# Performance work log

Measured on AMD Instinct MI355X. Metric: run time of the kernel, lower is better.

Reference implementation:

```python
import jax, jax.numpy as jnp
import numpy as np

N = 50000      # nodes
E = 800000     # edges
M = 1000000    # total subgraph membership rows
D = 128        # atom_fea_len
ED = 64        # nbr_fea_len
H = 8          # heads
C = D // H     # per-head dim


def _ln(x, g, b, eps=1e-5):
    mu = x.mean(-1, keepdims=True)
    var = ((x - mu) ** 2).mean(-1, keepdims=True)
    return (x - mu) / jnp.sqrt(var + eps) * g + b


def setup_inputs() -> dict:
    key = jax.random.key(0)
    ks = jax.random.split(key, 16)
    s = 0.05
    inp = {
        "x": jax.random.normal(ks[0], (N, D), jnp.float32),
        "edge_index": jax.random.randint(ks[1], (2, E), 0, N, jnp.int32),
        "edge_attr": jax.random.normal(ks[2], (E, ED), jnp.float32),
        "sub_nodes": jax.random.randint(ks[3], (M,), 0, N, jnp.int32),
        "sub_indicator": jax.random.randint(ks[4], (M,), 0, N, jnp.int32),
        # TransformerConv params (PyG: lin_query/key/value, lin_edge, lin_skip, all with bias)
        "Wq": jax.random.normal(ks[5], (D, D), jnp.float32) * s,
        "bq": jnp.zeros((D,), jnp.float32),
        "Wk": jax.random.normal(ks[6], (D, D), jnp.float32) * s,
        "bk": jnp.zeros((D,), jnp.float32),
        "Wv": jax.random.normal(ks[7], (D, D), jnp.float32) * s,
        "bv": jnp.zeros((D,), jnp.float32),
        "We": jax.random.normal(ks[8], (ED, D), jnp.float32) * s,
        "be": jnp.zeros((D,), jnp.float32),
        "Ws": jax.random.normal(ks[9], (D, D), jnp.float32) * s,
        "bs": jnp.zeros((D,), jnp.float32),
        # subgraph_norm
        "sn_g": jnp.ones((D,), jnp.float32),
        "sn_b": jnp.zeros((D,), jnp.float32),
        # subgraph_proj: Linear -> SiLU -> Linear
        "p1_w": jax.random.normal(ks[10], (D, D), jnp.float32) * s,
        "p1_b": jnp.zeros((D,), jnp.float32),
        "p2_w": jax.random.normal(ks[11], (D, D), jnp.float32) * s,
        "p2_b": jnp.zeros((D,), jnp.float32),
        # out_norm
        "on_g": jnp.ones((D,), jnp.float32),
        "on_b": jnp.zeros((D,), jnp.float32),
    }
    return inp


def reference(x, edge_index, edge_attr, sub_nodes, sub_indicator,
              Wq, bq, Wk, bk, Wv, bv, We, be, Ws, bs,
              sn_g, sn_b, p1_w, p1_b, p2_w, p2_b, on_g, on_b):
    n = x.shape[0]
    src, dst = edge_index[0], edge_index[1]  # messages flow src -> dst (PyG source_to_target)

    # ---- TransformerConv ----
    q = (x @ Wq + bq).reshape(n, H, C)
    k = (x @ Wk + bk).reshape(n, H, C)
    v = (x @ Wv + bv).reshape(n, H, C)
    e = (edge_attr @ We + be).reshape(-1, H, C)       # [E,H,C]
    ke = k[src] + e                                    # edge-conditioned keys
    ve = v[src] + e                                    # edge-conditioned values
    alpha = (q[dst] * ke).sum(-1) / jnp.sqrt(jnp.asarray(C, x.dtype))  # [E,H]
    # scatter-softmax over incoming edges of each dst node
    m = jax.ops.segment_max(alpha, dst, num_segments=n)               # [N,H]
    ea = jnp.exp(alpha - m[dst])
    denom = jax.ops.segment_sum(ea, dst, num_segments=n)              # [N,H]
    num = jax.ops.segment_sum(ea[:, :, None] * ve, dst, num_segments=n)  # [N,H,C]
    attn = num / jnp.where(denom > 0, denom, 1.0)[:, :, None]
    x_trans = attn.reshape(n, H * C) + (x @ Ws + bs)   # concat heads + root skip

    # ---- subgraph branch: gather -> LayerNorm -> MLP -> scatter-mean ----
    sx = x[sub_nodes]                                  # [M,D]
    sx = _ln(sx, sn_g, sn_b)
    sx = jax.nn.silu(sx @ p1_w + p1_b) @ p2_w + p2_b
    cnt = jax.ops.segment_sum(jnp.ones((sx.shape[0],), x.dtype), sub_indicator, num_segments=n)
    sub_x = jax.ops.segment_sum(sx, sub_indicator, num_segments=n) / jnp.maximum(cnt, 1.0)[:, None]

    # ---- combine (dropout is identity in eval) ----
    out = _ln(x + x_trans + sub_x, on_g, on_b)
    return jax.nn.silu(out)
```

## Files before the change

kernel.cpp:

```cpp
#include <hip/hip_runtime.h>
#include <math.h>

#define DD 128
#define EDD 64

typedef __attribute__((ext_vector_type(8))) short bf16x8;
typedef __attribute__((ext_vector_type(4))) float f32x4;

__device__ inline unsigned short f2bf(float f) {
    unsigned int u = __float_as_uint(f);
    u += 0x7FFFu + ((u >> 16) & 1u);
    return (unsigned short)(u >> 16);
}
__device__ inline unsigned int pack2bf16(float lo, float hi) {
    return (unsigned int)f2bf(lo) | ((unsigned int)f2bf(hi) << 16);
}
__device__ inline float bflo(unsigned int u) { return __uint_as_float(u << 16); }
__device__ inline float bfhi(unsigned int u) { return __uint_as_float(u & 0xffff0000u); }

__global__ __launch_bounds__(256) void packw_kernel(const float* __restrict__ w,
                                                    unsigned short* __restrict__ packed)
{
    int idx = blockIdx.x * 256 + threadIdx.x;
    if (idx >= DD * DD) return;
    int j    = idx & 7;
    int lane = (idx >> 3) & 63;
    int kt   = (idx >> 9) & 3;
    int ncf  = idx >> 11;
    int kk  = kt * 32 + (lane >> 4) * 8 + j;
    int col = ncf * 16 + (lane & 15);
    packed[idx] = f2bf(w[kk * DD + col]);
}

__device__ inline void gemm_b(const bf16x8 af[4][2], const unsigned short* __restrict__ packB,
                              int wc, int lane, f32x4 acc[2][4])
{
    #pragma unroll
    for (int i = 0; i < 2; i++)
        #pragma unroll
        for (int j = 0; j < 4; j++) acc[i][j] = (f32x4){0.f, 0.f, 0.f, 0.f};
    #pragma unroll
    for (int kt = 0; kt < 4; kt++) {
        #pragma unroll
        for (int nc = 0; nc < 4; nc++) {
            bf16x8 b = *(const bf16x8*)&packB[(((wc * 4 + nc) * 4 + kt) * 64 + lane) * 8];
            acc[0][nc] = __builtin_amdgcn_mfma_f32_16x16x32_bf16(af[kt][0], b, acc[0][nc], 0, 0, 0);
            acc[1][nc] = __builtin_amdgcn_mfma_f32_16x16x32_bf16(af[kt][1], b, acc[1][nc], 0, 0, 0);
        }
    }
}

__global__ __launch_bounds__(256, 4) void lin4_mfma_kernel(
    const float* __restrict__ x,
    const unsigned short* __restrict__ packBq, const float* __restrict__ bq,
    const unsigned short* __restrict__ packBk, const float* __restrict__ bk,
    const unsigned short* __restrict__ packBv, const float* __restrict__ bv,
    const unsigned short* __restrict__ packBs, const float* __restrict__ bs,
    const float* __restrict__ sn_g, const float* __restrict__ sn_b,
    float* __restrict__ q, unsigned short* __restrict__ kplane, unsigned short* __restrict__ vplane,
    float* __restrict__ pre, unsigned int* __restrict__ lnx, int N)
{
    __shared__ unsigned short sxs[64 * DD];
    int tid = threadIdx.x;
    int lane = tid & 63, wid = tid >> 6;
    size_t m0 = (size_t)blockIdx.x * 64;

    {
        float g0 = sn_g[2 * lane], g1 = sn_g[2 * lane + 1];
        float b0 = sn_b[2 * lane], b1 = sn_b[2 * lane + 1];
        #pragma unroll
        for (int r = 0; r < 16; r++) {
            int tr = wid * 16 + r;
            size_t row = m0 + tr;
            float v0 = 0.f, v1 = 0.f;
            if (row < (size_t)N) {
                float2 xv = *(const float2*)&x[row * DD + 2 * lane];
                v0 = xv.x; v1 = xv.y;
            }
            unsigned int uidx = ((unsigned)(tr * 64 + lane)) ^ (((unsigned)tr & 7u) << 2);
            ((unsigned int*)sxs)[uidx] = pack2bf16(v0, v1);
            float s1 = v0 + v1, s2 = v0 * v0 + v1 * v1;
            #pragma unroll
            for (int o = 32; o >= 1; o >>= 1) { s1 += __shfl_xor(s1, o); s2 += __shfl_xor(s2, o); }
            float mean = s1 * (1.f / DD);
            float var  = s2 * (1.f / DD) - mean * mean;
            float rs = rsqrtf(var + 1e-5f);
            if (row < (size_t)N)
                lnx[row * 64 + lane] = pack2bf16((v0 - mean) * rs * g0 + b0,
                                                 (v1 - mean) * rs * g1 + b1);
        }
    }
    __syncthreads();

    int wr = wid >> 1, wc = wid & 1;
    int rA = wr * 32 + (lane & 15);
    int kb = (lane >> 4) * 8;

    bf16x8 af[4][2];
    #pragma unroll
    for (int kt = 0; kt < 4; kt++) {
        int k0 = kt * 32 + kb;
        af[kt][0] = *(const bf16x8*)&sxs[((rA)      * DD + k0) ^ ((rA & 7) << 3)];
        int rA1 = rA + 16;
        af[kt][1] = *(const bf16x8*)&sxs[((rA1)     * DD + k0) ^ ((rA1 & 7) << 3)];
    }

    f32x4 acc[2][4];
    int colb = wc * 64 + (lane & 15);
    int jrow = (lane >> 4) * 4;

    gemm_b(af, packBq, wc, lane, acc);
    #pragma unroll
    for (int mrf = 0; mrf < 2; mrf++) {
        int rbase = wr * 32 + mrf * 16 + jrow;
        #pragma unroll
        for (int nc = 0; nc < 4; nc++) {
            int col = colb + nc * 16;
            float bias = bq[col];
            #pragma unroll
            for (int j = 0; j < 4; j++) {
                size_t row = m0 + rbase + j;
                if (row < (size_t)N) q[row * DD + col] = acc[mrf][nc][j] + bias;
            }
        }
    }
    gemm_b(af, packBk, wc, lane, acc);
    #pragma unroll
    for (int mrf = 0; mrf < 2; mrf++) {
        int rbase = wr * 32 + mrf * 16 + jrow;
        #pragma unroll
        for (int nc = 0; nc < 4; nc++) {
            int col = colb + nc * 16;
            float bias = bk[col];
            #pragma unroll
            for (int j = 0; j < 4; j++) {
                size_t row = m0 + rbase + j;
                if (row < (size_t)N) kplane[row * DD + col] = f2bf(acc[mrf][nc][j] + bias);
            }
        }
    }
    gemm_b(af, packBv, wc, lane, acc);
    #pragma unroll
    for (int mrf = 0; mrf < 2; mrf++) {
        int rbase = wr * 32 + mrf * 16 + jrow;
        #pragma unroll
        for (int nc = 0; nc < 4; nc++) {
            int col = colb + nc * 16;
            float bias = bv[col];
            #pragma unroll
            for (int j = 0; j < 4; j++) {
                size_t row = m0 + rbase + j;
                if (row < (size_t)N) vplane[row * DD + col] = f2bf(acc[mrf][nc][j] + bias);
            }
        }
    }
    gemm_b(af, packBs, wc, lane, acc);
    #pragma unroll
    for (int mrf = 0; mrf < 2; mrf++) {
        int rbase = wr * 32 + mrf * 16 + jrow;
        #pragma unroll
        for (int nc = 0; nc < 4; nc++) {
            int col = colb + nc * 16;
            float bias = bs[col];
            #pragma unroll
            for (int j = 0; j < 4; j++) {
                size_t row = m0 + rbase + j;
                if (row < (size_t)N)
                    pre[row * DD + col] = x[row * DD + col] + acc[mrf][nc][j] + bias;
            }
        }
    }
}

__global__ __launch_bounds__(256, 4) void mlpnode_kernel(
    const unsigned int* __restrict__ lnx,
    const unsigned short* __restrict__ packB1, const float* __restrict__ p1b,
    const unsigned short* __restrict__ packB2, const float* __restrict__ p2b,
    unsigned short* __restrict__ fnode, int N)
{
    __shared__ unsigned short sxs[64 * DD];
    int tid = threadIdx.x;
    int lane = tid & 63, wid = tid >> 6;
    size_t m0 = (size_t)blockIdx.x * 64;

    #pragma unroll
    for (int r = 0; r < 16; r++) {
        int tr = wid * 16 + r;
        size_t row = m0 + tr;
        unsigned int val = (row < (size_t)N) ? lnx[row * 64 + lane] : 0u;
        unsigned int uidx = ((unsigned)(tr * 64 + lane)) ^ (((unsigned)tr & 7u) << 2);
        ((unsigned int*)sxs)[uidx] = val;
    }
    __syncthreads();

    int wr = wid >> 1, wc = wid & 1;
    int rA = wr * 32 + (lane & 15);
    int kb = (lane >> 4) * 8;

    f32x4 acc[2][4];
    #pragma unroll
    for (int i = 0; i < 2; i++)
        #pragma unroll
        for (int j = 0; j < 4; j++) acc[i][j] = (f32x4){0.f, 0.f, 0.f, 0.f};
    #pragma unroll
    for (int kt = 0; kt < 4; kt++) {
        int k0 = kt * 32 + kb;
        bf16x8 a0 = *(const bf16x8*)&sxs[((rA)  * DD + k0) ^ ((rA & 7) << 3)];
        int rA1 = rA + 16;
        bf16x8 a1 = *(const bf16x8*)&sxs[((rA1) * DD + k0) ^ ((rA1 & 7) << 3)];
        #pragma unroll
        for (int nc = 0; nc < 4; nc++) {
            bf16x8 b = *(const bf16x8*)&packB1[(((wc * 4 + nc) * 4 + kt) * 64 + lane) * 8];
            acc[0][nc] = __builtin_amdgcn_mfma_f32_16x16x32_bf16(a0, b, acc[0][nc], 0, 0, 0);
            acc[1][nc] = __builtin_amdgcn_mfma_f32_16x16x32_bf16(a1, b, acc[1][nc], 0, 0, 0);
        }
    }
    __syncthreads();

    {
        float bias1[4];
        #pragma unroll
        for (int nc = 0; nc < 4; nc++) bias1[nc] = p1b[wc * 64 + nc * 16 + (lane & 15)];
        #pragma unroll
        for (int mrf = 0; mrf < 2; mrf++) {
            int rbase = wr * 32 + mrf * 16 + (lane >> 4) * 4;
            #pragma unroll
            for (int nc = 0; nc < 4; nc++) {
                int col = wc * 64 + nc * 16 + (lane & 15);
                #pragma unroll
                for (int j = 0; j < 4; j++) {
                    float h = acc[mrf][nc][j] + bias1[nc];
                    h = h / (1.f + __expf(-h));
                    int rr = rbase + j;
                    sxs[(rr * DD + col) ^ ((rr & 7) << 3)] = f2bf(h);
                }
            }
        }
    }
    __syncthreads();

    f32x4 acc2[2][4];
    #pragma unroll
    for (int i = 0; i < 2; i++)
        #pragma unroll
        for (int j = 0; j < 4; j++) acc2[i][j] = (f32x4){0.f, 0.f, 0.f, 0.f};
    #pragma unroll
    for (int kt = 0; kt < 4; kt++) {
        int k0 = kt * 32 + kb;
        bf16x8 a0 = *(const bf16x8*)&sxs[((rA)  * DD + k0) ^ ((rA & 7) << 3)];
        int rA1 = rA + 16;
        bf16x8 a1 = *(const bf16x8*)&sxs[((rA1) * DD + k0) ^ ((rA1 & 7) << 3)];
        #pragma unroll
        for (int nc = 0; nc < 4; nc++) {
            bf16x8 b = *(const bf16x8*)&packB2[(((wc * 4 + nc) * 4 + kt) * 64 + lane) * 8];
            acc2[0][nc] = __builtin_amdgcn_mfma_f32_16x16x32_bf16(a0, b, acc2[0][nc], 0, 0, 0);
            acc2[1][nc] = __builtin_amdgcn_mfma_f32_16x16x32_bf16(a1, b, acc2[1][nc], 0, 0, 0);
        }
    }

    {
        float bias2[4];
        #pragma unroll
        for (int nc = 0; nc < 4; nc++) bias2[nc] = p2b[wc * 64 + nc * 16 + (lane & 15)];
        #pragma unroll
        for (int mrf = 0; mrf < 2; mrf++) {
            int rbase = wr * 32 + mrf * 16 + (lane >> 4) * 4;
            #pragma unroll
            for (int nc = 0; nc < 4; nc++) {
                int col = wc * 64 + nc * 16 + (lane & 15);
                #pragma unroll
                for (int j = 0; j < 4; j++) {
                    size_t row = m0 + rbase + j;
                    if (row < (size_t)N)
                        fnode[row * DD + col] = f2bf(acc2[mrf][nc][j] + bias2[nc]);
                }
            }
        }
    }
}

__global__ void count_kernel(const int* __restrict__ idx, int n, int* __restrict__ cnt)
{
    int i = blockIdx.x * blockDim.x + threadIdx.x;
    int stride = gridDim.x * blockDim.x;
    for (; i < n; i += stride) atomicAdd(&cnt[idx[i]], 1);
}

__global__ __launch_bounds__(1024) void bscan_kernel(
    const int* __restrict__ inA, const int* __restrict__ inB,
    int* __restrict__ exA, int* __restrict__ exB,
    int* __restrict__ bsA, int* __restrict__ bsB, int N)
{
    const int* in = blockIdx.y ? inB : inA;
    int* ex = blockIdx.y ? exB : exA;
    int* bs = blockIdx.y ? bsB : bsA;
    __shared__ int s[1024];
    int tid = threadIdx.x;
    int i = blockIdx.x * 1024 + tid;
    int val = (i < N) ? in[i] : 0;
    s[tid] = val; __syncthreads();
    for (int off = 1; off < 1024; off <<= 1) {
        int t = (tid >= off) ? s[tid - off] : 0;
        __syncthreads();
        s[tid] += t;
        __syncthreads();
    }
    if (i < N) ex[i] = s[tid] - val;
    if (tid == 1023) bs[blockIdx.x] = s[1023];
}

__global__ void bsum_kernel(int* __restrict__ bsA, int* __restrict__ bsB,
                            int* __restrict__ indptrA, int* __restrict__ indptrB,
                            int nb, int N)
{
    int which = threadIdx.x;
    if (which < 2) {
        int* bs = which ? bsB : bsA;
        int* indptr = which ? indptrB : indptrA;
        int run = 0;
        for (int b = 0; b < nb; b++) { int v = bs[b]; bs[b] = run; run += v; }
        indptr[N] = run;
    }
}

__global__ void bfix_kernel(int* __restrict__ exA, int* __restrict__ fillA, const int* __restrict__ bsA,
                            int* __restrict__ exB, int* __restrict__ fillB, const int* __restrict__ bsB,
                            int N)
{
    int i = blockIdx.x * blockDim.x + threadIdx.x;
    if (i < N) {
        int vA = exA[i] + bsA[i >> 10];
        exA[i] = vA; fillA[i] = vA;
        int vB = exB[i] + bsB[i >> 10];
        exB[i] = vB; fillB[i] = vB;
    }
}

__global__ void escatter_kernel(const int* __restrict__ srcA, const int* __restrict__ dstA, int E,
                                int* __restrict__ fill, int2* __restrict__ spair)
{
    int i = blockIdx.x * blockDim.x + threadIdx.x;
    int stride = gridDim.x * blockDim.x;
    for (; i < E; i += stride) {
        int d = dstA[i];
        int pos = atomicAdd(&fill[d], 1);
        spair[pos] = make_int2(srcA[i], i);
    }
}

__global__ __launch_bounds__(256) void egather_kernel(
    const float* __restrict__ edge_attr, const int2* __restrict__ spair,
    unsigned int* __restrict__ ea16u, int E)
{
    size_t i = (size_t)blockIdx.x * blockDim.x + threadIdx.x;
    size_t stride = (size_t)gridDim.x * blockDim.x;
    size_t total = (size_t)E * 8;
    for (; i < total; i += stride) {
        size_t pos = i >> 3;
        int part = (int)(i & 7);
        int eid = spair[pos].y;
        const float4* s = (const float4*)&edge_attr[(size_t)eid * EDD + part * 8];
        float4 a = s[0], b = s[1];
        uint4 o;
        o.x = pack2bf16(a.x, a.y); o.y = pack2bf16(a.z, a.w);
        o.z = pack2bf16(b.x, b.y); o.w = pack2bf16(b.z, b.w);
        *(uint4*)&ea16u[pos * 32 + part * 4] = o;
    }
}

__global__ void sscatter_kernel(const int* __restrict__ sub_nodes, const int* __restrict__ sub_ind,
                                int M, int* __restrict__ sfill, int* __restrict__ snode)
{
    int i = blockIdx.x * blockDim.x + threadIdx.x;
    int stride = gridDim.x * blockDim.x;
    for (; i < M; i += stride) {
        int seg = sub_ind[i];
        int pos = atomicAdd(&sfill[seg], 1);
        snode[pos] = sub_nodes[i];
    }
}

__global__ __launch_bounds__(256) void qprep_kernel(
    const float* __restrict__ q, const float* __restrict__ We,
    unsigned int* __restrict__ qweU, int N)
{
    int tid = threadIdx.x;
    int wave = tid >> 6, lane = tid & 63;
    int n = blockIdx.x * 4 + wave;
    if (n >= N) return;
    int jj = lane & 7, g = lane >> 3;
    int hc0 = g * 16;
    const float4* qp = (const float4*)&q[(size_t)n * DD + hc0];
    float4 q0 = qp[0], q1 = qp[1], q2 = qp[2], q3 = qp[3];
    float qWe[8];
    #pragma unroll
    for (int r = 0; r < 8; r++) {
        const float4* wp = (const float4*)&We[(size_t)(8 * jj + r) * DD + hc0];
        float4 wa = wp[0], wb = wp[1], wc = wp[2], wd = wp[3];
        qWe[r] = q0.x * wa.x + q0.y * wa.y + q0.z * wa.z + q0.w * wa.w
               + q1.x * wb.x + q1.y * wb.y + q1.z * wb.z + q1.w * wb.w
               + q2.x * wc.x + q2.y * wc.y + q2.z * wc.z + q2.w * wc.w
               + q3.x * wd.x + q3.y * wd.y + q3.z * wd.z + q3.w * wd.w;
    }
    uint4 packed;
    packed.x = pack2bf16(qWe[0], qWe[1]);
    packed.y = pack2bf16(qWe[2], qWe[3]);
    packed.z = pack2bf16(qWe[4], qWe[5]);
    packed.w = pack2bf16(qWe[6], qWe[7]);
    *(uint4*)&qweU[(size_t)n * 256 + 4 * lane] = packed;
}

__global__ __launch_bounds__(256, 4) void attn_kernel(
    const float* __restrict__ q,
    const unsigned int* __restrict__ kplane32, const unsigned int* __restrict__ vplane32,
    const unsigned int* __restrict__ ea16u, const unsigned int* __restrict__ qweU,
    const float* __restrict__ We, const float* __restrict__ be,
    const int* __restrict__ indptr, const int2* __restrict__ spair,
    float* __restrict__ pre, int N)
{
    int tid = threadIdx.x;
    int wave = tid >> 6, lane = tid & 63;
    int n = blockIdx.x * 4 + wave;
    if (n >= N) return;

    int gbase = lane & 56;
    int jj = lane & 7;
    int c0 = lane * 2;

    float2 qv  = *(const float2*)&q[(size_t)n * DD + c0];
    float2 bev = *(const float2*)&be[c0];

    float t = qv.x * bev.x + qv.y * bev.y;
    t += __shfl_xor(t, 1); t += __shfl_xor(t, 2); t += __shfl_xor(t, 4);
    float qbe4 = t * 0.25f;

    uint4 qw = *(const uint4*)&qweU[(size_t)n * 256 + 4 * lane];
    float qwe0 = bflo(qw.x), qwe1 = bfhi(qw.x), qwe2 = bflo(qw.y), qwe3 = bfhi(qw.y);
    float qwe4 = bflo(qw.z), qwe5 = bfhi(qw.z), qwe6 = bflo(qw.w), qwe7 = bfhi(qw.w);

    int start = indptr[n], end = indptr[n + 1];
    float s = 0.f, av0 = 0.f, av1 = 0.f;
    float aea[8];
    #pragma unroll
    for (int r = 0; r < 8; r++) aea[r] = 0.f;

    int ii = start;
    for (; ii + 3 < end; ii += 4) {
        int2 se[4];
        #pragma unroll
        for (int u = 0; u < 4; u++) se[u] = spair[ii + u];
        uint4 ea[4];
        unsigned int ku[4], vu[4];
        #pragma unroll
        for (int u = 0; u < 4; u++) {
            ea[u] = *(const uint4*)&ea16u[(size_t)(ii + u) * 32 + jj * 4];
            ku[u] = kplane32[(size_t)se[u].x * 64 + lane];
            vu[u] = vplane32[(size_t)se[u].x * 64 + lane];
        }
        float p[4];
        #pragma unroll
        for (int u = 0; u < 4; u++) {
            float part = qv.x * bflo(ku[u]) + qv.y * bfhi(ku[u])
                       + bflo(ea[u].x) * qwe0 + bfhi(ea[u].x) * qwe1
                       + bflo(ea[u].y) * qwe2 + bfhi(ea[u].y) * qwe3
                       + bflo(ea[u].z) * qwe4 + bfhi(ea[u].z) * qwe5
                       + bflo(ea[u].w) * qwe6 + bfhi(ea[u].w) * qwe7;
            part += __shfl_xor(part, 1);
            part += __shfl_xor(part, 2);
            part += __shfl_xor(part, 4);
            p[u] = __expf(part * 0.25f + qbe4);
        }
        #pragma unroll
        for (int u = 0; u < 4; u++) {
            s += p[u];
            av0 += p[u] * bflo(vu[u]);
            av1 += p[u] * bfhi(vu[u]);
            aea[0] += p[u] * bflo(ea[u].x); aea[1] += p[u] * bfhi(ea[u].x);
            aea[2] += p[u] * bflo(ea[u].y); aea[3] += p[u] * bfhi(ea[u].y);
            aea[4] += p[u] * bflo(ea[u].z); aea[5] += p[u] * bfhi(ea[u].z);
            aea[6] += p[u] * bflo(ea[u].w); aea[7] += p[u] * bfhi(ea[u].w);
        }
    }
    for (; ii < end; ii++) {
        int2 se = spair[ii];
        uint4 ea = *(const uint4*)&ea16u[(size_t)ii * 32 + jj * 4];
        unsigned int ku = kplane32[(size_t)se.x * 64 + lane];
        unsigned int vu = vplane32[(size_t)se.x * 64 + lane];
        float part = qv.x * bflo(ku) + qv.y * bfhi(ku)
                   + bflo(ea.x) * qwe0 + bfhi(ea.x) * qwe1
                   + bflo(ea.y) * qwe2 + bfhi(ea.y) * qwe3
                   + bflo(ea.z) * qwe4 + bfhi(ea.z) * qwe5
                   + bflo(ea.w) * qwe6 + bfhi(ea.w) * qwe7;
        part += __shfl_xor(part, 1);
        part += __shfl_xor(part, 2);
        part += __shfl_xor(part, 4);
        float p = __expf(part * 0.25f + qbe4);
        s += p;
        av0 += p * bflo(vu);
        av1 += p * bfhi(vu);
        aea[0] += p * bflo(ea.x); aea[1] += p * bfhi(ea.x);
        aea[2] += p * bflo(ea.y); aea[3] += p * bfhi(ea.y);
        aea[4] += p * bflo(ea.z); aea[5] += p * bfhi(ea.z);
        aea[6] += p * bflo(ea.w); aea[7] += p * bfhi(ea.w);
    }

    if (end > start) {
        float inv = 1.f / s;
        float oe0 = 0.f, oe1 = 0.f;
        #pragma unroll
        for (int m = 0; m < 8; m++) {
            #pragma unroll
            for (int r = 0; r < 8; r++) {
                float a = __shfl(aea[r], gbase + m);
                float2 w = *(const float2*)&We[(size_t)(8 * m + r) * DD + c0];
                oe0 += a * w.x;
                oe1 += a * w.y;
            }
        }
        size_t o = (size_t)n * DD + c0;
        pre[o]     += (av0 + oe0) * inv + bev.x;
        pre[o + 1] += (av1 + oe1) * inv + bev.y;
    }
}

__global__ __launch_bounds__(256) void final2_kernel(
    const float* __restrict__ pre, const unsigned int* __restrict__ fnodeU,
    const int* __restrict__ sindptr, const int* __restrict__ snode,
    const float* __restrict__ on_g, const float* __restrict__ on_b,
    float* __restrict__ out, int N)
{
    int tid = threadIdx.x;
    int wave = tid >> 6, lane = tid & 63;
    int n = blockIdx.x * 4 + wave;
    if (n >= N) return;
    int c0 = 2 * lane;

    int start = sindptr[n], end = sindptr[n + 1];
    float sum0 = 0.f, sum1 = 0.f;
    int ii = start;
    for (; ii + 3 < end; ii += 4) {
        int n0 = snode[ii], n1 = snode[ii + 1], n2 = snode[ii + 2], n3 = snode[ii + 3];
        unsigned int u0 = fnodeU[(size_t)n0 * 64 + lane];
        unsigned int u1 = fnodeU[(size_t)n1 * 64 + lane];
        unsigned int u2 = fnodeU[(size_t)n2 * 64 + lane];
        unsigned int u3 = fnodeU[(size_t)n3 * 64 + lane];
        sum0 += bflo(u0) + bflo(u1) + bflo(u2) + bflo(u3);
        sum1 += bfhi(u0) + bfhi(u1) + bfhi(u2) + bfhi(u3);
    }
    for (; ii < end; ii++) {
        unsigned int u = fnodeU[(size_t)snode[ii] * 64 + lane];
        sum0 += bflo(u);
        sum1 += bfhi(u);
    }
    float inv = 1.f / fmaxf((float)(end - start), 1.f);

    float2 pv = *(const float2*)&pre[(size_t)n * DD + c0];
    float v0 = pv.x + sum0 * inv;
    float v1 = pv.y + sum1 * inv;

    float s1 = v0 + v1, s2 = v0 * v0 + v1 * v1;
    #pragma unroll
    for (int off = 32; off >= 1; off >>= 1) { s1 += __shfl_xor(s1, off); s2 += __shfl_xor(s2, off); }
    float mean = s1 * (1.f / DD);
    float var  = s2 * (1.f / DD) - mean * mean;
    float rs = rsqrtf(var + 1e-5f);

    float2 gv = *(const float2*)&on_g[c0];
    float2 bv = *(const float2*)&on_b[c0];
    float ov0 = (v0 - mean) * rs * gv.x + bv.x;
    float ov1 = (v1 - mean) * rs * gv.y + bv.y;
    float2 res;
    res.x = ov0 / (1.f + __expf(-ov0));
    res.y = ov1 / (1.f + __expf(-ov1));
    *(float2*)&out[(size_t)n * DD + c0] = res;
}

extern "C" void kernel_launch(void* const* d_in, const int* in_sizes, int n_in,
                              void* d_out, int out_size, void* d_ws, size_t ws_size,
                              hipStream_t stream)
{
    const float* x         = (const float*)d_in[0];
    const int*   edge_index= (const int*)  d_in[1];
    const float* edge_attr = (const float*)d_in[2];
    const int*   sub_nodes = (const int*)  d_in[3];
    const int*   sub_ind   = (const int*)  d_in[4];
    const float* Wq = (const float*)d_in[5];  const float* bq = (const float*)d_in[6];
    const float* Wk = (const float*)d_in[7];  const float* bk = (const float*)d_in[8];
    const float* Wv = (const float*)d_in[9];  const float* bv = (const float*)d_in[10];
    const float* We = (const float*)d_in[11]; const float* be = (const float*)d_in[12];
    const float* Ws = (const float*)d_in[13]; const float* bs = (const float*)d_in[14];
    const float* sn_g = (const float*)d_in[15]; const float* sn_b = (const float*)d_in[16];
    const float* p1w = (const float*)d_in[17]; const float* p1b = (const float*)d_in[18];
    const float* p2w = (const float*)d_in[19]; const float* p2b = (const float*)d_in[20];
    const float* on_g = (const float*)d_in[21]; const float* on_b = (const float*)d_in[22];

    int N = in_sizes[0] / DD;
    int E = in_sizes[1] / 2;
    int M = in_sizes[3];
    float* out = (float*)d_out;

    unsigned short* packB1 = (unsigned short*)d_ws;
    unsigned short* packB2 = packB1 + DD * DD;
    unsigned short* packBq = packB2 + DD * DD;
    unsigned short* packBk = packBq + DD * DD;
    unsigned short* packBv = packBk + DD * DD;
    unsigned short* packBs = packBv + DD * DD;
    size_t ND = (size_t)N * DD;
    float* q     = (float*)(packBs + DD * DD);
    unsigned short* kplane = (unsigned short*)(q + ND);
    unsigned short* vplane = kplane + ND;
    float* pre   = (float*)(vplane + ND);
    unsigned int* qweU  = (unsigned int*)(pre + ND);
    unsigned int* lnx   = qweU + (size_t)N * 256;
    unsigned int* fnode = lnx + (size_t)N * 64;
    unsigned int* ea16u = fnode + (size_t)N * 64;
    int2* spair  = (int2*)(ea16u + (size_t)E * 32);
    int* indptr  = (int*)(spair + E);
    int* fill    = indptr + (N + 1);
    int* deg     = fill + N;
    int* cnt     = deg + N;
    int* sindptr = cnt + N;
    int* sfill   = sindptr + (N + 1);
    int* snode   = sfill + N;
    int* bsA     = snode + M;
    int* bsB     = bsA + 64;

    const int* srcA = edge_index;
    const int* dstA = edge_index + E;

    int nb = (N + 1023) / 1024;

    hipMemsetAsync(deg, 0, (size_t)N * sizeof(int), stream);
    hipMemsetAsync(cnt, 0, (size_t)N * sizeof(int), stream);

    packw_kernel<<<64, 256, 0, stream>>>(p1w, packB1);
    packw_kernel<<<64, 256, 0, stream>>>(p2w, packB2);
    packw_kernel<<<64, 256, 0, stream>>>(Wq, packBq);
    packw_kernel<<<64, 256, 0, stream>>>(Wk, packBk);
    packw_kernel<<<64, 256, 0, stream>>>(Wv, packBv);
    packw_kernel<<<64, 256, 0, stream>>>(Ws, packBs);

    lin4_mfma_kernel<<<(N + 63) / 64, 256, 0, stream>>>(x, packBq, bq, packBk, bk, packBv, bv,
                                                        packBs, bs, sn_g, sn_b,
                                                        q, kplane, vplane, pre, lnx, N);
    mlpnode_kernel<<<(N + 63) / 64, 256, 0, stream>>>(lnx, packB1, p1b, packB2, p2b,
                                                      (unsigned short*)fnode, N);
    count_kernel<<<2048, 256, 0, stream>>>(dstA, E, deg);
    count_kernel<<<2048, 256, 0, stream>>>(sub_ind, M, cnt);
    {
        dim3 g(nb, 2);
        bscan_kernel<<<g, 1024, 0, stream>>>(deg, cnt, indptr, sindptr, bsA, bsB, N);
    }
    bsum_kernel<<<1, 64, 0, stream>>>(bsA, bsB, indptr, sindptr, nb, N);
    bfix_kernel<<<(N + 255) / 256, 256, 0, stream>>>(indptr, fill, bsA, sindptr, sfill, bsB, N);
    escatter_kernel<<<2048, 256, 0, stream>>>(srcA, dstA, E, fill, spair);
    egather_kernel<<<4096, 256, 0, stream>>>(edge_attr, spair, ea16u, E);
    sscatter_kernel<<<2048, 256, 0, stream>>>(sub_nodes, sub_ind, M, sfill, snode);
    qprep_kernel<<<(N + 3) / 4, 256, 0, stream>>>(q, We, qweU, N);
    attn_kernel<<<(N + 3) / 4, 256, 0, stream>>>(q, (const unsigned int*)kplane,
                                                 (const unsigned int*)vplane, ea16u, qweU,
                                                 We, be, indptr, spair, pre, N);
    final2_kernel<<<(N + 3) / 4, 256, 0, stream>>>(pre, fnode, sindptr, snode, on_g, on_b, out, N);
}
```

Before: 805.8 us.

## Split per-node edge and subgraph loops across two waves; gather edge attrs in source order

The attention and final kernels now assign two waves to each node. Each wave processes half of the node's incoming edges or subgraph members, and the partial sums are combined through shared memory before the epilogue. This doubles memory-level parallelism for these latency-bound gather loops, at the cost of a block-wide sync and extra LDS traffic. The edge scatter also records a perm array, so the edge-attribute conversion reads edge_attr sequentially and scatters the writes, instead of gathering reads through spair. The perm buffer is appended after bsB in the workspace.

```diff
diff --git a/kernel.cpp b/kernel.cpp
--- a/kernel.cpp
+++ b/kernel.cpp
@@ -337,7 +337,8 @@
 }
 
 __global__ void escatter_kernel(const int* __restrict__ srcA, const int* __restrict__ dstA, int E,
-                                int* __restrict__ fill, int2* __restrict__ spair)
+                                int* __restrict__ fill, int2* __restrict__ spair,
+                                int* __restrict__ perm)
 {
     int i = blockIdx.x * blockDim.x + threadIdx.x;
     int stride = gridDim.x * blockDim.x;
@@ -345,26 +346,27 @@
         int d = dstA[i];
         int pos = atomicAdd(&fill[d], 1);
         spair[pos] = make_int2(srcA[i], i);
+        perm[i] = pos;
     }
 }
 
 __global__ __launch_bounds__(256) void egather_kernel(
-    const float* __restrict__ edge_attr, const int2* __restrict__ spair,
+    const float* __restrict__ edge_attr, const int* __restrict__ perm,
     unsigned int* __restrict__ ea16u, int E)
 {
     size_t i = (size_t)blockIdx.x * blockDim.x + threadIdx.x;
     size_t stride = (size_t)gridDim.x * blockDim.x;
     size_t total = (size_t)E * 8;
     for (; i < total; i += stride) {
-        size_t pos = i >> 3;
+        size_t eid = i >> 3;
         int part = (int)(i & 7);
-        int eid = spair[pos].y;
-        const float4* s = (const float4*)&edge_attr[(size_t)eid * EDD + part * 8];
+        const float4* s = (const float4*)&edge_attr[eid * EDD + part * 8];
         float4 a = s[0], b = s[1];
+        int pos = perm[eid];
         uint4 o;
         o.x = pack2bf16(a.x, a.y); o.y = pack2bf16(a.z, a.w);
         o.z = pack2bf16(b.x, b.y); o.w = pack2bf16(b.z, b.w);
-        *(uint4*)&ea16u[pos * 32 + part * 4] = o;
+        *(uint4*)&ea16u[(size_t)pos * 32 + part * 4] = o;
     }
 }
 
@@ -410,7 +412,7 @@
     *(uint4*)&qweU[(size_t)n * 256 + 4 * lane] = packed;
 }
 
-__global__ __launch_bounds__(256, 4) void attn_kernel(
+__global__ __launch_bounds__(512, 4) void attn_kernel(
     const float* __restrict__ q,
     const unsigned int* __restrict__ kplane32, const unsigned int* __restrict__ vplane32,
     const unsigned int* __restrict__ ea16u, const unsigned int* __restrict__ qweU,
@@ -418,34 +420,43 @@
     const int* __restrict__ indptr, const int2* __restrict__ spair,
     float* __restrict__ pre, int N)
 {
+    __shared__ float comb[4][11][64];
     int tid = threadIdx.x;
     int wave = tid >> 6, lane = tid & 63;
-    int n = blockIdx.x * 4 + wave;
-    if (n >= N) return;
+    int slot = wave >> 1, half = wave & 1;
+    int n = blockIdx.x * 4 + slot;
+    bool valid = (n < N);
+    int nn = valid ? n : 0;
 
     int gbase = lane & 56;
     int jj = lane & 7;
     int c0 = lane * 2;
 
-    float2 qv  = *(const float2*)&q[(size_t)n * DD + c0];
+    float2 qv  = *(const float2*)&q[(size_t)nn * DD + c0];
     float2 bev = *(const float2*)&be[c0];
 
     float t = qv.x * bev.x + qv.y * bev.y;
     t += __shfl_xor(t, 1); t += __shfl_xor(t, 2); t += __shfl_xor(t, 4);
     float qbe4 = t * 0.25f;
 
-    uint4 qw = *(const uint4*)&qweU[(size_t)n * 256 + 4 * lane];
+    uint4 qw = *(const uint4*)&qweU[(size_t)nn * 256 + 4 * lane];
     float qwe0 = bflo(qw.x), qwe1 = bfhi(qw.x), qwe2 = bflo(qw.y), qwe3 = bfhi(qw.y);
     float qwe4 = bflo(qw.z), qwe5 = bfhi(qw.z), qwe6 = bflo(qw.w), qwe7 = bfhi(qw.w);
 
-    int start = indptr[n], end = indptr[n + 1];
+    int start = valid ? indptr[n] : 0;
+    int end   = valid ? indptr[n + 1] : 0;
+    int len = end - start;
+    int mid = start + (len >> 1);
+    int lo = half ? mid : start;
+    int hi = half ? end : mid;
+
     float s = 0.f, av0 = 0.f, av1 = 0.f;
     float aea[8];
     #pragma unroll
     for (int r = 0; r < 8; r++) aea[r] = 0.f;
 
-    int ii = start;
-    for (; ii + 3 < end; ii += 4) {
+    int ii = lo;
+    for (; ii + 3 < hi; ii += 4) {
         int2 se[4];
         #pragma unroll
         for (int u = 0; u < 4; u++) se[u] = spair[ii + u];
@@ -481,7 +492,7 @@
             aea[6] += p[u] * bflo(ea[u].w); aea[7] += p[u] * bfhi(ea[u].w);
         }
     }
-    for (; ii < end; ii++) {
+    for (; ii < hi; ii++) {
         int2 se = spair[ii];
         uint4 ea = *(const uint4*)&ea16u[(size_t)ii * 32 + jj * 4];
         unsigned int ku = kplane32[(size_t)se.x * 64 + lane];
@@ -504,7 +515,22 @@
         aea[6] += p * bflo(ea.w); aea[7] += p * bfhi(ea.w);
     }
 
-    if (end > start) {
+    if (half == 1) {
+        comb[slot][0][lane] = s;
+        comb[slot][1][lane] = av0;
+        comb[slot][2][lane] = av1;
+        #pragma unroll
+        for (int r = 0; r < 8; r++) comb[slot][3 + r][lane] = aea[r];
+    }
+    __syncthreads();
+
+    if (half == 0 && valid && end > start) {
+        s   += comb[slot][0][lane];
+        av0 += comb[slot][1][lane];
+        av1 += comb[slot][2][lane];
+        #pragma unroll
+        for (int r = 0; r < 8; r++) aea[r] += comb[slot][3 + r][lane];
+
         float inv = 1.f / s;
         float oe0 = 0.f, oe1 = 0.f;
         #pragma unroll
@@ -523,22 +549,30 @@
     }
 }
 
-__global__ __launch_bounds__(256) void final2_kernel(
+__global__ __launch_bounds__(512, 4) void final2_kernel(
     const float* __restrict__ pre, const unsigned int* __restrict__ fnodeU,
     const int* __restrict__ sindptr, const int* __restrict__ snode,
     const float* __restrict__ on_g, const float* __restrict__ on_b,
     float* __restrict__ out, int N)
 {
+    __shared__ float comb[4][2][64];
     int tid = threadIdx.x;
     int wave = tid >> 6, lane = tid & 63;
-    int n = blockIdx.x * 4 + wave;
-    if (n >= N) return;
+    int slot = wave >> 1, half = wave & 1;
+    int n = blockIdx.x * 4 + slot;
+    bool valid = (n < N);
     int c0 = 2 * lane;
 
-    int start = sindptr[n], end = sindptr[n + 1];
+    int start = valid ? sindptr[n] : 0;
+    int end   = valid ? sindptr[n + 1] : 0;
+    int len = end - start;
+    int mid = start + (len >> 1);
+    int lo = half ? mid : start;
+    int hi = half ? end : mid;
+
     float sum0 = 0.f, sum1 = 0.f;
-    int ii = start;
-    for (; ii + 3 < end; ii += 4) {
+    int ii = lo;
+    for (; ii + 3 < hi; ii += 4) {
         int n0 = snode[ii], n1 = snode[ii + 1], n2 = snode[ii + 2], n3 = snode[ii + 3];
         unsigned int u0 = fnodeU[(size_t)n0 * 64 + lane];
         unsigned int u1 = fnodeU[(size_t)n1 * 64 + lane];
@@ -547,32 +581,43 @@
         sum0 += bflo(u0) + bflo(u1) + bflo(u2) + bflo(u3);
         sum1 += bfhi(u0) + bfhi(u1) + bfhi(u2) + bfhi(u3);
     }
-    for (; ii < end; ii++) {
+    for (; ii < hi; ii++) {
         unsigned int u = fnodeU[(size_t)snode[ii] * 64 + lane];
         sum0 += bflo(u);
         sum1 += bfhi(u);
     }
-    float inv = 1.f / fmaxf((float)(end - start), 1.f);
-
-    float2 pv = *(const float2*)&pre[(size_t)n * DD + c0];
-    float v0 = pv.x + sum0 * inv;
-    float v1 = pv.y + sum1 * inv;
-
-    float s1 = v0 + v1, s2 = v0 * v0 + v1 * v1;
-    #pragma unroll
-    for (int off = 32; off >= 1; off >>= 1) { s1 += __shfl_xor(s1, off); s2 += __shfl_xor(s2, off); }
-    float mean = s1 * (1.f / DD);
-    float var  = s2 * (1.f / DD) - mean * mean;
-    float rs = rsqrtf(var + 1e-5f);
-
-    float2 gv = *(const float2*)&on_g[c0];
-    float2 bv = *(const float2*)&on_b[c0];
-    float ov0 = (v0 - mean) * rs * gv.x + bv.x;
-    float ov1 = (v1 - mean) * rs * gv.y + bv.y;
-    float2 res;
-    res.x = ov0 / (1.f + __expf(-ov0));
-    res.y = ov1 / (1.f + __expf(-ov1));
-    *(float2*)&out[(size_t)n * DD + c0] = res;
+
+    if (half == 1) {
+        comb[slot][0][lane] = sum0;
+        comb[slot][1][lane] = sum1;
+    }
+    __syncthreads();
+
+    if (half == 0 && valid) {
+        sum0 += comb[slot][0][lane];
+        sum1 += comb[slot][1][lane];
+        float inv = 1.f / fmaxf((float)len, 1.f);
+
+        float2 pv = *(const float2*)&pre[(size_t)n * DD + c0];
+        float v0 = pv.x + sum0 * inv;
+        float v1 = pv.y + sum1 * inv;
+
+        float s1 = v0 + v1, s2 = v0 * v0 + v1 * v1;
+        #pragma unroll
+        for (int off = 32; off >= 1; off >>= 1) { s1 += __shfl_xor(s1, off); s2 += __shfl_xor(s2, off); }
+        float mean = s1 * (1.f / DD);
+        float var  = s2 * (1.f / DD) - mean * mean;
+        float rs = rsqrtf(var + 1e-5f);
+
+        float2 gv = *(const float2*)&on_g[c0];
+        float2 bv = *(const float2*)&on_b[c0];
+        float ov0 = (v0 - mean) * rs * gv.x + bv.x;
+        float ov1 = (v1 - mean) * rs * gv.y + bv.y;
+        float2 res;
+        res.x = ov0 / (1.f + __expf(-ov0));
+        res.y = ov1 / (1.f + __expf(-ov1));
+        *(float2*)&out[(size_t)n * DD + c0] = res;
+    }
 }
 
 extern "C" void kernel_launch(void* const* d_in, const int* in_sizes, int n_in,
@@ -624,6 +669,7 @@
     int* snode   = sfill + N;
     int* bsA     = snode + M;
     int* bsB     = bsA + 64;
+    int* perm    = bsB + 64;
 
     const int* srcA = edge_index;
     const int* dstA = edge_index + E;
@@ -653,12 +699,12 @@
     }
     bsum_kernel<<<1, 64, 0, stream>>>(bsA, bsB, indptr, sindptr, nb, N);
     bfix_kernel<<<(N + 255) / 256, 256, 0, stream>>>(indptr, fill, bsA, sindptr, sfill, bsB, N);
-    escatter_kernel<<<2048, 256, 0, stream>>>(srcA, dstA, E, fill, spair);
-    egather_kernel<<<4096, 256, 0, stream>>>(edge_attr, spair, ea16u, E);
+    escatter_kernel<<<2048, 256, 0, stream>>>(srcA, dstA, E, fill, spair, perm);
+    egather_kernel<<<4096, 256, 0, stream>>>(edge_attr, perm, ea16u, E);
     sscatter_kernel<<<2048, 256, 0, stream>>>(sub_nodes, sub_ind, M, sfill, snode);
     qprep_kernel<<<(N + 3) / 4, 256, 0, stream>>>(q, We, qweU, N);
-    attn_kernel<<<(N + 3) / 4, 256, 0, stream>>>(q, (const unsigned int*)kplane,
+    attn_kernel<<<(N + 3) / 4, 512, 0, stream>>>(q, (const unsigned int*)kplane,
                                                  (const unsigned int*)vplane, ea16u, qweU,
                                                  We, be, indptr, spair, pre, N);
-    final2_kernel<<<(N + 3) / 4, 256, 0, stream>>>(pre, fnode, sindptr, snode, on_g, on_b, out, N);
-}
+    final2_kernel<<<(N + 3) / 4, 512, 0, stream>>>(pre, fnode, sindptr, snode, on_g, on_b, out, N);
+}
```

Result: slower. 884.7 us (+9.8%).

## Fuse preprocessing kernels, convert edge attrs unsorted, and process attention nodes by degree

Applied to the files above, without the earlier changes.

Merges the six weight-pack launches into one and fuses the counting passes with a bf16 conversion of edge_attr in original edge order. This drops the separate sorted-gather pass, and attention now reads edge attributes indirectly through the stored edge id. It also buckets nodes by in-degree (descending) and has the attention kernel visit nodes in that order to balance wave work. The costs are scattered ea16u reads in attention, an extra bucket scan, and a permutation array.

```diff
diff --git a/kernel.cpp b/kernel.cpp
--- a/kernel.cpp
+++ b/kernel.cpp
@@ -18,9 +18,15 @@
 __device__ inline float bflo(unsigned int u) { return __uint_as_float(u << 16); }
 __device__ inline float bfhi(unsigned int u) { return __uint_as_float(u & 0xffff0000u); }
 
-__global__ __launch_bounds__(256) void packw_kernel(const float* __restrict__ w,
-                                                    unsigned short* __restrict__ packed)
-{
+__global__ __launch_bounds__(256) void packw6_kernel(
+    const float* __restrict__ w0, const float* __restrict__ w1, const float* __restrict__ w2,
+    const float* __restrict__ w3, const float* __restrict__ w4, const float* __restrict__ w5,
+    unsigned short* __restrict__ packed)
+{
+    int which = blockIdx.y;
+    const float* w = which == 0 ? w0 : which == 1 ? w1 : which == 2 ? w2
+                   : which == 3 ? w3 : which == 4 ? w4 : w5;
+    unsigned short* pk = packed + (size_t)which * DD * DD;
     int idx = blockIdx.x * 256 + threadIdx.x;
     if (idx >= DD * DD) return;
     int j    = idx & 7;
@@ -29,7 +35,7 @@
     int ncf  = idx >> 11;
     int kk  = kt * 32 + (lane >> 4) * 8 + j;
     int col = ncf * 16 + (lane & 15);
-    packed[idx] = f2bf(w[kk * DD + col]);
+    pk[idx] = f2bf(w[kk * DD + col]);
 }
 
 __device__ inline void gemm_b(const bf16x8 af[4][2], const unsigned short* __restrict__ packB,
@@ -279,11 +285,26 @@
     }
 }
 
-__global__ void count_kernel(const int* __restrict__ idx, int n, int* __restrict__ cnt)
-{
-    int i = blockIdx.x * blockDim.x + threadIdx.x;
-    int stride = gridDim.x * blockDim.x;
-    for (; i < n; i += stride) atomicAdd(&cnt[idx[i]], 1);
+__global__ __launch_bounds__(256) void prep1_kernel(
+    const int* __restrict__ dstA, const int* __restrict__ sub_ind,
+    const float* __restrict__ edge_attr, unsigned int* __restrict__ ea16u,
+    int* __restrict__ deg, int* __restrict__ cnt, int E, int M)
+{
+    size_t i = (size_t)blockIdx.x * blockDim.x + threadIdx.x;
+    size_t stride = (size_t)gridDim.x * blockDim.x;
+    size_t total = (size_t)E * 8;
+    for (size_t t = i; t < total; t += stride) {
+        size_t eid = t >> 3;
+        int part = (int)(t & 7);
+        const float4* s = (const float4*)&edge_attr[eid * EDD + part * 8];
+        float4 a = s[0], b = s[1];
+        uint4 o;
+        o.x = pack2bf16(a.x, a.y); o.y = pack2bf16(a.z, a.w);
+        o.z = pack2bf16(b.x, b.y); o.w = pack2bf16(b.z, b.w);
+        *(uint4*)&ea16u[eid * 32 + part * 4] = o;
+        if (part == 0) atomicAdd(&deg[dstA[eid]], 1);
+        if (t < (size_t)M) atomicAdd(&cnt[sub_ind[t]], 1);
+    }
 }
 
 __global__ __launch_bounds__(1024) void bscan_kernel(
@@ -325,7 +346,7 @@
 
 __global__ void bfix_kernel(int* __restrict__ exA, int* __restrict__ fillA, const int* __restrict__ bsA,
                             int* __restrict__ exB, int* __restrict__ fillB, const int* __restrict__ bsB,
-                            int N)
+                            const int* __restrict__ deg, int* __restrict__ dbuck, int N)
 {
     int i = blockIdx.x * blockDim.x + threadIdx.x;
     if (i < N) {
@@ -333,50 +354,53 @@
         exA[i] = vA; fillA[i] = vA;
         int vB = exB[i] + bsB[i >> 10];
         exB[i] = vB; fillB[i] = vB;
-    }
-}
-
-__global__ void escatter_kernel(const int* __restrict__ srcA, const int* __restrict__ dstA, int E,
-                                int* __restrict__ fill, int2* __restrict__ spair)
+        int b = deg[i]; if (b > 1023) b = 1023;
+        atomicAdd(&dbuck[b], 1);
+    }
+}
+
+__global__ __launch_bounds__(1024) void dsortscan_kernel(const int* __restrict__ dbuck,
+                                                         int* __restrict__ dfill)
+{
+    __shared__ int s[1024];
+    int tid = threadIdx.x;
+    int val = dbuck[1023 - tid];
+    s[tid] = val; __syncthreads();
+    for (int off = 1; off < 1024; off <<= 1) {
+        int t = (tid >= off) ? s[tid - off] : 0;
+        __syncthreads();
+        s[tid] += t;
+        __syncthreads();
+    }
+    dfill[1023 - tid] = s[tid] - val;
+}
+
+__global__ void prep2_kernel(
+    const int* __restrict__ srcA, const int* __restrict__ dstA, int E,
+    int* __restrict__ fill, int2* __restrict__ spair,
+    const int* __restrict__ sub_nodes, const int* __restrict__ sub_ind, int M,
+    int* __restrict__ sfill, int* __restrict__ snode,
+    const int* __restrict__ deg, int* __restrict__ dfill, int* __restrict__ norder, int N)
 {
     int i = blockIdx.x * blockDim.x + threadIdx.x;
     int stride = gridDim.x * blockDim.x;
-    for (; i < E; i += stride) {
-        int d = dstA[i];
-        int pos = atomicAdd(&fill[d], 1);
-        spair[pos] = make_int2(srcA[i], i);
-    }
-}
-
-__global__ __launch_bounds__(256) void egather_kernel(
-    const float* __restrict__ edge_attr, const int2* __restrict__ spair,
-    unsigned int* __restrict__ ea16u, int E)
-{
-    size_t i = (size_t)blockIdx.x * blockDim.x + threadIdx.x;
-    size_t stride = (size_t)gridDim.x * blockDim.x;
-    size_t total = (size_t)E * 8;
-    for (; i < total; i += stride) {
-        size_t pos = i >> 3;
-        int part = (int)(i & 7);
-        int eid = spair[pos].y;
-        const float4* s = (const float4*)&edge_attr[(size_t)eid * EDD + part * 8];
-        float4 a = s[0], b = s[1];
-        uint4 o;
-        o.x = pack2bf16(a.x, a.y); o.y = pack2bf16(a.z, a.w);
-        o.z = pack2bf16(b.x, b.y); o.w = pack2bf16(b.z, b.w);
-        *(uint4*)&ea16u[pos * 32 + part * 4] = o;
-    }
-}
-
-__global__ void sscatter_kernel(const int* __restrict__ sub_nodes, const int* __restrict__ sub_ind,
-                                int M, int* __restrict__ sfill, int* __restrict__ snode)
-{
-    int i = blockIdx.x * blockDim.x + threadIdx.x;
-    int stride = gridDim.x * blockDim.x;
-    for (; i < M; i += stride) {
-        int seg = sub_ind[i];
-        int pos = atomicAdd(&sfill[seg], 1);
-        snode[pos] = sub_nodes[i];
+    int total = M > E ? M : E;
+    for (int t = i; t < total; t += stride) {
+        if (t < E) {
+            int d = dstA[t];
+            int pos = atomicAdd(&fill[d], 1);
+            spair[pos] = make_int2(srcA[t], t);
+        }
+        if (t < M) {
+            int seg = sub_ind[t];
+            int pos = atomicAdd(&sfill[seg], 1);
+            snode[pos] = sub_nodes[t];
+        }
+        if (t < N) {
+            int b = deg[t]; if (b > 1023) b = 1023;
+            int pos = atomicAdd(&dfill[b], 1);
+            norder[pos] = t;
+        }
     }
 }
 
@@ -416,12 +440,14 @@
     const unsigned int* __restrict__ ea16u, const unsigned int* __restrict__ qweU,
     const float* __restrict__ We, const float* __restrict__ be,
     const int* __restrict__ indptr, const int2* __restrict__ spair,
+    const int* __restrict__ norder,
     float* __restrict__ pre, int N)
 {
     int tid = threadIdx.x;
     int wave = tid >> 6, lane = tid & 63;
-    int n = blockIdx.x * 4 + wave;
-    if (n >= N) return;
+    int slot = blockIdx.x * 4 + wave;
+    if (slot >= N) return;
+    int n = norder[slot];
 
     int gbase = lane & 56;
     int jj = lane & 7;
@@ -453,7 +479,7 @@
         unsigned int ku[4], vu[4];
         #pragma unroll
         for (int u = 0; u < 4; u++) {
-            ea[u] = *(const uint4*)&ea16u[(size_t)(ii + u) * 32 + jj * 4];
+            ea[u] = *(const uint4*)&ea16u[(size_t)se[u].y * 32 + jj * 4];
             ku[u] = kplane32[(size_t)se[u].x * 64 + lane];
             vu[u] = vplane32[(size_t)se[u].x * 64 + lane];
         }
@@ -483,7 +509,7 @@
     }
     for (; ii < end; ii++) {
         int2 se = spair[ii];
-        uint4 ea = *(const uint4*)&ea16u[(size_t)ii * 32 + jj * 4];
+        uint4 ea = *(const uint4*)&ea16u[(size_t)se.y * 32 + jj * 4];
         unsigned int ku = kplane32[(size_t)se.x * 64 + lane];
         unsigned int vu = vplane32[(size_t)se.x * 64 + lane];
         float part = qv.x * bflo(ku) + qv.y * bfhi(ku)
@@ -599,7 +625,8 @@
     int M = in_sizes[3];
     float* out = (float*)d_out;
 
-    unsigned short* packB1 = (unsigned short*)d_ws;
+    unsigned short* packAll = (unsigned short*)d_ws;
+    unsigned short* packB1 = packAll;
     unsigned short* packB2 = packB1 + DD * DD;
     unsigned short* packBq = packB2 + DD * DD;
     unsigned short* packBk = packBq + DD * DD;
@@ -619,46 +646,47 @@
     int* fill    = indptr + (N + 1);
     int* deg     = fill + N;
     int* cnt     = deg + N;
-    int* sindptr = cnt + N;
+    int* dbuck   = cnt + N;
+    int* sindptr = dbuck + 1024;
     int* sfill   = sindptr + (N + 1);
     int* snode   = sfill + N;
     int* bsA     = snode + M;
     int* bsB     = bsA + 64;
+    int* dfill   = bsB + 64;
+    int* norder  = dfill + 1024;
 
     const int* srcA = edge_index;
     const int* dstA = edge_index + E;
 
     int nb = (N + 1023) / 1024;
 
-    hipMemsetAsync(deg, 0, (size_t)N * sizeof(int), stream);
-    hipMemsetAsync(cnt, 0, (size_t)N * sizeof(int), stream);
-
-    packw_kernel<<<64, 256, 0, stream>>>(p1w, packB1);
-    packw_kernel<<<64, 256, 0, stream>>>(p2w, packB2);
-    packw_kernel<<<64, 256, 0, stream>>>(Wq, packBq);
-    packw_kernel<<<64, 256, 0, stream>>>(Wk, packBk);
-    packw_kernel<<<64, 256, 0, stream>>>(Wv, packBv);
-    packw_kernel<<<64, 256, 0, stream>>>(Ws, packBs);
+    hipMemsetAsync(deg, 0, ((size_t)2 * N + 1024) * sizeof(int), stream);
+
+    {
+        dim3 g(64, 6);
+        packw6_kernel<<<g, 256, 0, stream>>>(p1w, p2w, Wq, Wk, Wv, Ws, packAll);
+    }
 
     lin4_mfma_kernel<<<(N + 63) / 64, 256, 0, stream>>>(x, packBq, bq, packBk, bk, packBv, bv,
                                                         packBs, bs, sn_g, sn_b,
                                                         q, kplane, vplane, pre, lnx, N);
     mlpnode_kernel<<<(N + 63) / 64, 256, 0, stream>>>(lnx, packB1, p1b, packB2, p2b,
                                                       (unsigned short*)fnode, N);
-    count_kernel<<<2048, 256, 0, stream>>>(dstA, E, deg);
-    count_kernel<<<2048, 256, 0, stream>>>(sub_ind, M, cnt);
+    prep1_kernel<<<4096, 256, 0, stream>>>(dstA, sub_ind, edge_attr, ea16u, deg, cnt, E, M);
     {
         dim3 g(nb, 2);
         bscan_kernel<<<g, 1024, 0, stream>>>(deg, cnt, indptr, sindptr, bsA, bsB, N);
     }
     bsum_kernel<<<1, 64, 0, stream>>>(bsA, bsB, indptr, sindptr, nb, N);
-    bfix_kernel<<<(N + 255) / 256, 256, 0, stream>>>(indptr, fill, bsA, sindptr, sfill, bsB, N);
-    escatter_kernel<<<2048, 256, 0, stream>>>(srcA, dstA, E, fill, spair);
-    egather_kernel<<<4096, 256, 0, stream>>>(edge_attr, spair, ea16u, E);
-    sscatter_kernel<<<2048, 256, 0, stream>>>(sub_nodes, sub_ind, M, sfill, snode);
+    bfix_kernel<<<(N + 255) / 256, 256, 0, stream>>>(indptr, fill, bsA, sindptr, sfill, bsB,
+                                                     deg, dbuck, N);
+    dsortscan_kernel<<<1, 1024, 0, stream>>>(dbuck, dfill);
+    prep2_kernel<<<2048, 256, 0, stream>>>(srcA, dstA, E, fill, spair,
+                                           sub_nodes, sub_ind, M, sfill, snode,
+                                           deg, dfill, norder, N);
     qprep_kernel<<<(N + 3) / 4, 256, 0, stream>>>(q, We, qweU, N);
     attn_kernel<<<(N + 3) / 4, 256, 0, stream>>>(q, (const unsigned int*)kplane,
                                                  (const unsigned int*)vplane, ea16u, qweU,
-                                                 We, be, indptr, spair, pre, N);
+                                                 We, be, indptr, spair, norder, pre, N);
     final2_kernel<<<(N + 3) / 4, 256, 0, stream>>>(pre, fnode, sindptr, snode, on_g, on_b, out, N);
 }
```

New measurement: 1.047 ms. 29.9% more time.
